# Optimization experiments

Measured on AMD Instinct MI355X. Metric: run time of the kernel, lower is better.

## Reference

```python
import jax, jax.numpy as jnp
import numpy as np

LOG2 = float(np.log(2.0))

def ssp(x):
    # ShiftedSoftplus: softplus(x) - log(2)
    return jax.nn.softplus(x) - LOG2

B, N, F, R, P = 8, 1000, 128, 20, 512000  # batch, atoms, n_atom_basis=n_filters, n_rbf, n_pairs

def setup_inputs() -> dict:
    key = jax.random.key(0)
    ks = jax.random.split(key, 14)
    inv = lambda d: 1.0 / np.sqrt(d)
    return {
        "x": jax.random.normal(ks[0], (B, N, F), dtype=jnp.float32),
        "f_ij": jax.random.normal(ks[1], (P, R), dtype=jnp.float32),
        "idx_i": jax.random.randint(ks[2], (P,), 0, B * N, dtype=jnp.int32),
        "idx_j": jax.random.randint(ks[3], (P,), 0, B * N, dtype=jnp.int32),
        "rcut_ij": jax.random.uniform(ks[4], (P,), dtype=jnp.float32),
        # input_to_feature: Linear(F, F)
        "W_in": jax.random.normal(ks[5], (F, F), dtype=jnp.float32) * inv(F),
        "b_in": jnp.zeros((F,), dtype=jnp.float32),
        # filter_network: Linear(R, F) -> SSP -> Linear(F, F)
        "Wf1": jax.random.normal(ks[6], (R, F), dtype=jnp.float32) * inv(R),
        "bf1": jnp.zeros((F,), dtype=jnp.float32),
        "Wf2": jax.random.normal(ks[7], (F, F), dtype=jnp.float32) * inv(F),
        "bf2": jnp.zeros((F,), dtype=jnp.float32),
        # feature_to_output: Linear(F, F) -> SSP -> Linear(F, F)
        "Wo1": jax.random.normal(ks[8], (F, F), dtype=jnp.float32) * inv(F),
        "bo1": jnp.zeros((F,), dtype=jnp.float32),
        "Wo2": jax.random.normal(ks[9], (F, F), dtype=jnp.float32) * inv(F),
        "bo2": jnp.zeros((F,), dtype=jnp.float32),
    }

def reference(x, f_ij, idx_i, idx_j, rcut_ij,
              W_in, b_in, Wf1, bf1, Wf2, bf2, Wo1, bo1, Wo2, bo2):
    batch, n_atoms = x.shape[0], x.shape[1]
    # input_to_feature
    h = (x @ W_in + b_in).reshape(batch * n_atoms, -1)      # [B*N, F]
    # filter network on radial basis, modulated by cutoff
    Wij = ssp(f_ij @ Wf1 + bf1) @ Wf2 + bf2                 # [P, F]
    Wij = Wij * rcut_ij[:, None]
    # gather neighbor features, elementwise filter, scatter-add to center atom
    x_ij = h[idx_j] * Wij                                   # [P, F]
    agg = jax.ops.segment_sum(x_ij, idx_i, num_segments=batch * n_atoms)  # [B*N, F]
    # feature_to_output
    out = ssp(agg @ Wo1 + bo1) @ Wo2 + bo2
    return out.reshape(batch, n_atoms, 128)
```

## Files before the change

kernel.cpp:

```cpp
#include <hip/hip_runtime.h>
#include <math.h>

#define FDIM 128
#define RDIM 20
#define BN   8000
#define NPAIR 512000
#define PB   64
#define ROWS 8

typedef __attribute__((ext_vector_type(8))) short short8v;
typedef __attribute__((ext_vector_type(4))) float float4v;

__device__ __forceinline__ float sspf_fast(float x) {
    return fmaxf(x, 0.0f) + __logf(1.0f + __expf(-fabsf(x))) - 0.69314718055994531f;
}
__device__ __forceinline__ float sspf(float x) {
    return fmaxf(x, 0.0f) + log1pf(expf(-fabsf(x))) - 0.69314718055994531f;
}

__device__ __forceinline__ unsigned short f2bf(float x) {
    union { float f; unsigned u; } v; v.f = x;
    unsigned r = (v.u + 0x7FFFu + ((v.u >> 16) & 1u)) >> 16;
    return (unsigned short)r;
}

__global__ __launch_bounds__(256) void hist_kernel(
    const int* __restrict__ idx_i, int* __restrict__ cnt)
{
    const int p = blockIdx.x * 256 + threadIdx.x;
    if (p < NPAIR) atomicAdd(&cnt[idx_i[p]], 1);
}

__global__ __launch_bounds__(1024) void scan_kernel(
    const int* __restrict__ cnt, int* __restrict__ cursor)
{
    __shared__ int part[1024];
    const int t = threadIdx.x;
    int v[8]; int sum = 0;
    #pragma unroll
    for (int k = 0; k < 8; ++k) {
        const int i = t * 8 + k;
        const int c = (i < BN) ? cnt[i] : 0;
        v[k] = sum; sum += c;
    }
    part[t] = sum;
    __syncthreads();
    for (int off = 1; off < 1024; off <<= 1) {
        const int x = (t >= off) ? part[t - off] : 0;
        __syncthreads();
        part[t] += x;
        __syncthreads();
    }
    const int base = (t == 0) ? 0 : part[t - 1];
    #pragma unroll
    for (int k = 0; k < 8; ++k) {
        const int i = t * 8 + k;
        if (i < BN) cursor[i] = base + v[k];
    }
}

__global__ __launch_bounds__(256) void scatter_kernel(
    const int* __restrict__ idx_i, int* __restrict__ cursor, int* __restrict__ perm)
{
    const int p = blockIdx.x * 256 + threadIdx.x;
    if (p < NPAIR) {
        const int pos = atomicAdd(&cursor[idx_i[p]], 1);
        perm[pos] = p;
    }
}

template<bool SSP, bool BF16OUT>
__global__ __launch_bounds__(256) void rowgemm_kernel(
    const float* __restrict__ A, const float* __restrict__ W,
    const float* __restrict__ bias, void* __restrict__ Cv)
{
    __shared__ float rowlds[16 * 128];
    const int tid = threadIdx.x;
    const int blk = blockIdx.x;
    for (int s = tid; s < 16 * 128; s += 256)
        rowlds[s] = A[blk * 16 * 128 + s];
    __syncthreads();

    const int lane = tid & 63;
    const int wave = tid >> 6;
    const float b0 = bias[lane];
    const float b1 = bias[64 + lane];
    float acc[4][2];
    #pragma unroll
    for (int rr = 0; rr < 4; ++rr) { acc[rr][0] = b0; acc[rr][1] = b1; }

    #pragma unroll 4
    for (int m = 0; m < 128; ++m) {
        const float w0 = W[m * 128 + lane];
        const float w1 = W[m * 128 + 64 + lane];
        #pragma unroll
        for (int rr = 0; rr < 4; ++rr) {
            const float av = rowlds[(wave * 4 + rr) * 128 + m];
            acc[rr][0] = fmaf(av, w0, acc[rr][0]);
            acc[rr][1] = fmaf(av, w1, acc[rr][1]);
        }
    }

    #pragma unroll
    for (int rr = 0; rr < 4; ++rr) {
        const int p = blk * 16 + wave * 4 + rr;
        float v0 = acc[rr][0], v1 = acc[rr][1];
        if (SSP) { v0 = sspf(v0); v1 = sspf(v1); }
        if (BF16OUT) {
            unsigned short* C = (unsigned short*)Cv;
            C[p * 128 + lane]      = f2bf(v0);
            C[p * 128 + 64 + lane] = f2bf(v1);
        } else {
            float* C = (float*)Cv;
            C[p * 128 + lane]      = v0;
            C[p * 128 + 64 + lane] = v1;
        }
    }
}

__global__ __launch_bounds__(256) void pairs_mfma_agg(
    const float* __restrict__ f_ij, const int* __restrict__ idx_i,
    const int* __restrict__ idx_j, const float* __restrict__ rcut,
    const float* __restrict__ Wf1, const float* __restrict__ bf1,
    const float* __restrict__ Wf2, const float* __restrict__ bf2,
    const unsigned short* __restrict__ h2, const int* __restrict__ rowEnd,
    const int* __restrict__ perm, float* __restrict__ agg)
{
    __shared__ unsigned short xt[64 * 128];
    __shared__ int   rrs[PB];
    __shared__ int   jjs[PB];
    __shared__ float rcs[PB];

    const int tid = threadIdx.x;
    const int w   = tid >> 6;
    const int l   = tid & 63;
    const int l15 = l & 15;
    const int l4  = l >> 4;
    const int swz = (l15 & 7) << 4;

    const int row0 = blockIdx.x * ROWS;
    const int s0 = (row0 == 0) ? 0 : rowEnd[row0 - 1];
    const int s1 = rowEnd[row0 + ROWS - 1];

    short8v wf1a[2];
    #pragma unroll
    for (int kt2 = 0; kt2 < 2; ++kt2) {
        const int ck = w * 32 + kt2 * 16 + l15;
        #pragma unroll
        for (int e = 0; e < 8; ++e) {
            const int r = l4 * 8 + e;
            const float val = (r < RDIM) ? Wf1[r * 128 + ck] : 0.0f;
            wf1a[kt2][e] = (short)f2bf(val);
        }
    }
    short8v wf2a[2][4];
    #pragma unroll
    for (int mt = 0; mt < 2; ++mt) {
        const int c = w * 32 + mt * 16 + l15;
        #pragma unroll
        for (int ks = 0; ks < 4; ++ks) {
            #pragma unroll
            for (int e = 0; e < 8; ++e) {
                const int k = ks * 32 + l4 * 8 + e;
                wf2a[mt][ks][e] = (short)f2bf(Wf2[k * 128 + c]);
            }
        }
    }
    float b1v[2][4], b2v[2][4];
    #pragma unroll
    for (int t = 0; t < 2; ++t)
        #pragma unroll
        for (int j = 0; j < 4; ++j) {
            b1v[t][j] = bf1[w * 32 + t * 16 + l4 * 4 + j];
            b2v[t][j] = bf2[w * 32 + t * 16 + l4 * 4 + j];
        }

    float4v accD[2];
    accD[0] = float4v{0.f, 0.f, 0.f, 0.f};
    accD[1] = float4v{0.f, 0.f, 0.f, 0.f};

    for (int s = s0; s < s1; s += PB) {
        __syncthreads();

        if (tid < PB) {
            const int q  = s + tid;
            const int qc = q < s1 ? q : s1 - 1;
            const int pid = perm[qc];
            rrs[tid] = idx_i[pid] - row0;
            jjs[tid] = idx_j[pid];
            rcs[tid] = (q < s1) ? rcut[pid] : 0.0f;
        }

        short8v ffr[4];
        #pragma unroll
        for (int nt = 0; nt < 4; ++nt) {
            const int q = s + nt * 16 + l15;
            const int pid = perm[q < s1 ? q : s1 - 1];
            const float* fb = &f_ij[(size_t)pid * RDIM];
            float4 fa = {0.f, 0.f, 0.f, 0.f}, fc = {0.f, 0.f, 0.f, 0.f};
            if (l4 < 3) fa = *(const float4*)(fb + l4 * 8);
            if (l4 < 2) fc = *(const float4*)(fb + l4 * 8 + 4);
            ffr[nt][0] = (short)f2bf(fa.x); ffr[nt][1] = (short)f2bf(fa.y);
            ffr[nt][2] = (short)f2bf(fa.z); ffr[nt][3] = (short)f2bf(fa.w);
            ffr[nt][4] = (short)f2bf(fc.x); ffr[nt][5] = (short)f2bf(fc.y);
            ffr[nt][6] = (short)f2bf(fc.z); ffr[nt][7] = (short)f2bf(fc.w);
        }
        __syncthreads();

        unsigned long long hvb[4][2];
        #pragma unroll
        for (int nt = 0; nt < 4; ++nt) {
            const int gj = jjs[nt * 16 + l15] << 7;
            hvb[nt][0] = *(const unsigned long long*)&h2[gj + w * 32 + l4 * 4];
            hvb[nt][1] = *(const unsigned long long*)&h2[gj + w * 32 + 16 + l4 * 4];
        }

        #pragma unroll
        for (int kt2 = 0; kt2 < 2; ++kt2) {
            #pragma unroll
            for (int nt = 0; nt < 4; ++nt) {
                float4v acc1 = {0.f, 0.f, 0.f, 0.f};
                acc1 = __builtin_amdgcn_mfma_f32_16x16x32_bf16(wf1a[kt2], ffr[nt], acc1, 0, 0, 0);
                unsigned short pk[4];
                #pragma unroll
                for (int j = 0; j < 4; ++j)
                    pk[j] = f2bf(sspf_fast(acc1[j] + b1v[kt2][j]));
                const int row = nt * 16 + l15;
                const int byte = row * 256 + ((w * 64 + kt2 * 32 + l4 * 8) ^ swz);
                *(unsigned long long*)((char*)xt + byte) =
                    (unsigned long long)pk[0] | ((unsigned long long)pk[1] << 16) |
                    ((unsigned long long)pk[2] << 32) | ((unsigned long long)pk[3] << 48);
            }
        }
        __syncthreads();

        float4v a2[2][4];
        #pragma unroll
        for (int mt = 0; mt < 2; ++mt)
            #pragma unroll
            for (int nt = 0; nt < 4; ++nt)
                a2[mt][nt] = float4v{0.f, 0.f, 0.f, 0.f};

        #pragma unroll
        for (int ks = 0; ks < 4; ++ks) {
            short8v bfr[4];
            #pragma unroll
            for (int nt = 0; nt < 4; ++nt) {
                const int row = nt * 16 + l15;
                const int byte = row * 256 + ((ks * 64 + l4 * 16) ^ swz);
                bfr[nt] = *(const short8v*)((const char*)xt + byte);
            }
            #pragma unroll
            for (int mt = 0; mt < 2; ++mt)
                #pragma unroll
                for (int nt = 0; nt < 4; ++nt)
                    a2[mt][nt] = __builtin_amdgcn_mfma_f32_16x16x32_bf16(
                        wf2a[mt][ks], bfr[nt], a2[mt][nt], 0, 0, 0);
        }
        __syncthreads();

        #pragma unroll
        for (int nt = 0; nt < 4; ++nt) {
            const int p = nt * 16 + l15;
            const float r = rcs[p];
            #pragma unroll
            for (int mt = 0; mt < 2; ++mt) {
                #pragma unroll
                for (int j = 0; j < 4; ++j) {
                    const int c = w * 32 + mt * 16 + l4 * 4 + j;
                    const float hf = __uint_as_float(
                        (unsigned)((hvb[nt][mt] >> (16 * j)) & 0xFFFFULL) << 16);
                    const float xv = hf * ((a2[mt][nt][j] + b2v[mt][j]) * r);
                    const int byte = c * 128 + ((p * 2) ^ ((c & 7) << 4));
                    *(unsigned short*)((char*)xt + byte) = f2bf(xv);
                }
            }
        }
        __syncthreads();

        #pragma unroll
        for (int ks = 0; ks < 2; ++ks) {
            short8v sfr;
            #pragma unroll
            for (int e = 0; e < 8; ++e) {
                const int pr = ks * 32 + l4 * 8 + e;
                sfr[e] = (rrs[pr] == l15) ? (short)0x3F80 : (short)0;
            }
            #pragma unroll
            for (int mt = 0; mt < 2; ++mt) {
                const int c = w * 32 + mt * 16 + l15;
                const int byte = c * 128 + ((ks * 64 + l4 * 16) ^ swz);
                const short8v xfr = *(const short8v*)((const char*)xt + byte);
                accD[mt] = __builtin_amdgcn_mfma_f32_16x16x32_bf16(xfr, sfr, accD[mt], 0, 0, 0);
            }
        }
    }

    if (l15 < ROWS) {
        #pragma unroll
        for (int mt = 0; mt < 2; ++mt) {
            float4 v;
            v.x = accD[mt][0]; v.y = accD[mt][1]; v.z = accD[mt][2]; v.w = accD[mt][3];
            *(float4*)&agg[(size_t)(row0 + l15) * 128 + w * 32 + mt * 16 + l4 * 4] = v;
        }
    }
}

extern "C" void kernel_launch(void* const* d_in, const int* in_sizes, int n_in,
                              void* d_out, int out_size, void* d_ws, size_t ws_size,
                              hipStream_t stream) {
    const float* x     = (const float*)d_in[0];
    const float* f_ij  = (const float*)d_in[1];
    const int*   idx_i = (const int*)  d_in[2];
    const int*   idx_j = (const int*)  d_in[3];
    const float* rcut  = (const float*)d_in[4];
    const float* W_in  = (const float*)d_in[5];
    const float* b_in  = (const float*)d_in[6];
    const float* Wf1   = (const float*)d_in[7];
    const float* bf1   = (const float*)d_in[8];
    const float* Wf2   = (const float*)d_in[9];
    const float* bf2   = (const float*)d_in[10];
    const float* Wo1   = (const float*)d_in[11];
    const float* bo1   = (const float*)d_in[12];
    const float* Wo2   = (const float*)d_in[13];
    const float* bo2   = (const float*)d_in[14];
    float* out = (float*)d_out;

    unsigned short* h2 = (unsigned short*)d_ws;
    float* agg = (float*)((char*)d_ws + 2048000);
    float* t1  = (float*)((char*)d_ws + 2048000 + 4096000);
    int* perm   = (int*)t1;
    int* cnt    = (int*)((char*)t1 + (size_t)NPAIR * 4);
    int* cursor = cnt + 8001;

    hipMemsetAsync(cnt, 0, (BN + 1) * sizeof(int), stream);
    hist_kernel<<<NPAIR / 256, 256, 0, stream>>>(idx_i, cnt);
    scan_kernel<<<1, 1024, 0, stream>>>(cnt, cursor);
    scatter_kernel<<<NPAIR / 256, 256, 0, stream>>>(idx_i, cursor, perm);

    rowgemm_kernel<false, true><<<BN / 16, 256, 0, stream>>>(x, W_in, b_in, h2);

    pairs_mfma_agg<<<BN / ROWS, 256, 0, stream>>>(
        f_ij, idx_i, idx_j, rcut, Wf1, bf1, Wf2, bf2, h2, cursor, perm, agg);

    rowgemm_kernel<true,  false><<<BN / 16, 256, 0, stream>>>(agg, Wo1, bo1, t1);
    rowgemm_kernel<false, false><<<BN / 16, 256, 0, stream>>>(t1, Wo2, bo2, out);
}
```

Before: 238.0 us.

## Split pair-kernel LDS buffers, drop barriers, restructure filter loop, use packed bf16 conversion

The pair kernel now uses separate LDS buffers for the filter activations and the gathered products. Because each wave reads only the product columns it wrote itself, two __syncthreads per tile can be removed. The second filter GEMM now loops over the output tile outer-most, gathering h2 per tile, so fewer accumulators and neighbour values are live at once. Launch bounds request 4 blocks per CU. The hand-written bf16 rounding is replaced with the HIP intrinsic conversions, including a packed two-value variant. The trade-off is higher LDS use per block, which may limit how many blocks actually fit per CU.

```diff
diff --git a/kernel.cpp b/kernel.cpp
--- a/kernel.cpp
+++ b/kernel.cpp
@@ -1,4 +1,5 @@
 #include <hip/hip_runtime.h>
+#include <hip/hip_bf16.h>
 #include <math.h>
 
 #define FDIM 128
@@ -18,10 +19,15 @@
     return fmaxf(x, 0.0f) + log1pf(expf(-fabsf(x))) - 0.69314718055994531f;
 }
 
-__device__ __forceinline__ unsigned short f2bf(float x) {
-    union { float f; unsigned u; } v; v.f = x;
-    unsigned r = (v.u + 0x7FFFu + ((v.u >> 16) & 1u)) >> 16;
-    return (unsigned short)r;
+__device__ __forceinline__ unsigned short bfs(float a) {
+    union { __hip_bfloat16 h; unsigned short u; } v;
+    v.h = __float2bfloat16(a);
+    return v.u;
+}
+__device__ __forceinline__ unsigned pkbf(float a, float b) {
+    union { __hip_bfloat162 h; unsigned u; } v;
+    v.h = __float22bfloat162_rn(make_float2(a, b));
+    return v.u;
 }
 
 __global__ __launch_bounds__(256) void hist_kernel(
@@ -108,8 +114,8 @@
         if (SSP) { v0 = sspf(v0); v1 = sspf(v1); }
         if (BF16OUT) {
             unsigned short* C = (unsigned short*)Cv;
-            C[p * 128 + lane]      = f2bf(v0);
-            C[p * 128 + 64 + lane] = f2bf(v1);
+            C[p * 128 + lane]      = bfs(v0);
+            C[p * 128 + 64 + lane] = bfs(v1);
         } else {
             float* C = (float*)Cv;
             C[p * 128 + lane]      = v0;
@@ -118,7 +124,7 @@
     }
 }
 
-__global__ __launch_bounds__(256) void pairs_mfma_agg(
+__global__ __launch_bounds__(256, 4) void pairs_v7(
     const float* __restrict__ f_ij, const int* __restrict__ idx_i,
     const int* __restrict__ idx_j, const float* __restrict__ rcut,
     const float* __restrict__ Wf1, const float* __restrict__ bf1,
@@ -126,7 +132,8 @@
     const unsigned short* __restrict__ h2, const int* __restrict__ rowEnd,
     const int* __restrict__ perm, float* __restrict__ agg)
 {
-    __shared__ unsigned short xt[64 * 128];
+    __shared__ unsigned short act[64 * 128];
+    __shared__ unsigned short xbuf[128 * 64];
     __shared__ int   rrs[PB];
     __shared__ int   jjs[PB];
     __shared__ float rcs[PB];
@@ -150,7 +157,7 @@
         for (int e = 0; e < 8; ++e) {
             const int r = l4 * 8 + e;
             const float val = (r < RDIM) ? Wf1[r * 128 + ck] : 0.0f;
-            wf1a[kt2][e] = (short)f2bf(val);
+            wf1a[kt2][e] = (short)bfs(val);
         }
     }
     short8v wf2a[2][4];
@@ -162,7 +169,7 @@
             #pragma unroll
             for (int e = 0; e < 8; ++e) {
                 const int k = ks * 32 + l4 * 8 + e;
-                wf2a[mt][ks][e] = (short)f2bf(Wf2[k * 128 + c]);
+                wf2a[mt][ks][e] = (short)bfs(Wf2[k * 128 + c]);
             }
         }
     }
@@ -200,20 +207,12 @@
             float4 fa = {0.f, 0.f, 0.f, 0.f}, fc = {0.f, 0.f, 0.f, 0.f};
             if (l4 < 3) fa = *(const float4*)(fb + l4 * 8);
             if (l4 < 2) fc = *(const float4*)(fb + l4 * 8 + 4);
-            ffr[nt][0] = (short)f2bf(fa.x); ffr[nt][1] = (short)f2bf(fa.y);
-            ffr[nt][2] = (short)f2bf(fa.z); ffr[nt][3] = (short)f2bf(fa.w);
-            ffr[nt][4] = (short)f2bf(fc.x); ffr[nt][5] = (short)f2bf(fc.y);
-            ffr[nt][6] = (short)f2bf(fc.z); ffr[nt][7] = (short)f2bf(fc.w);
-        }
-        __syncthreads();
-
-        unsigned long long hvb[4][2];
-        #pragma unroll
-        for (int nt = 0; nt < 4; ++nt) {
-            const int gj = jjs[nt * 16 + l15] << 7;
-            hvb[nt][0] = *(const unsigned long long*)&h2[gj + w * 32 + l4 * 4];
-            hvb[nt][1] = *(const unsigned long long*)&h2[gj + w * 32 + 16 + l4 * 4];
-        }
+            union { unsigned u[4]; short8v v; } pk;
+            pk.u[0] = pkbf(fa.x, fa.y); pk.u[1] = pkbf(fa.z, fa.w);
+            pk.u[2] = pkbf(fc.x, fc.y); pk.u[3] = pkbf(fc.z, fc.w);
+            ffr[nt] = pk.v;
+        }
+        __syncthreads();
 
         #pragma unroll
         for (int kt2 = 0; kt2 < 2; ++kt2) {
@@ -221,62 +220,64 @@
             for (int nt = 0; nt < 4; ++nt) {
                 float4v acc1 = {0.f, 0.f, 0.f, 0.f};
                 acc1 = __builtin_amdgcn_mfma_f32_16x16x32_bf16(wf1a[kt2], ffr[nt], acc1, 0, 0, 0);
-                unsigned short pk[4];
-                #pragma unroll
-                for (int j = 0; j < 4; ++j)
-                    pk[j] = f2bf(sspf_fast(acc1[j] + b1v[kt2][j]));
+                const unsigned lo = pkbf(sspf_fast(acc1[0] + b1v[kt2][0]),
+                                         sspf_fast(acc1[1] + b1v[kt2][1]));
+                const unsigned hi = pkbf(sspf_fast(acc1[2] + b1v[kt2][2]),
+                                         sspf_fast(acc1[3] + b1v[kt2][3]));
                 const int row = nt * 16 + l15;
                 const int byte = row * 256 + ((w * 64 + kt2 * 32 + l4 * 8) ^ swz);
-                *(unsigned long long*)((char*)xt + byte) =
-                    (unsigned long long)pk[0] | ((unsigned long long)pk[1] << 16) |
-                    ((unsigned long long)pk[2] << 32) | ((unsigned long long)pk[3] << 48);
-            }
-        }
-        __syncthreads();
-
-        float4v a2[2][4];
-        #pragma unroll
-        for (int mt = 0; mt < 2; ++mt)
-            #pragma unroll
-            for (int nt = 0; nt < 4; ++nt)
-                a2[mt][nt] = float4v{0.f, 0.f, 0.f, 0.f};
-
-        #pragma unroll
-        for (int ks = 0; ks < 4; ++ks) {
-            short8v bfr[4];
+                *(unsigned long long*)((char*)act + byte) =
+                    (unsigned long long)lo | ((unsigned long long)hi << 32);
+            }
+        }
+        __syncthreads();
+
+        #pragma unroll
+        for (int mt = 0; mt < 2; ++mt) {
+            unsigned long long hv[4];
             #pragma unroll
             for (int nt = 0; nt < 4; ++nt) {
-                const int row = nt * 16 + l15;
-                const int byte = row * 256 + ((ks * 64 + l4 * 16) ^ swz);
-                bfr[nt] = *(const short8v*)((const char*)xt + byte);
-            }
-            #pragma unroll
-            for (int mt = 0; mt < 2; ++mt)
+                const int gj = jjs[nt * 16 + l15] << 7;
+                hv[nt] = *(const unsigned long long*)&h2[gj + w * 32 + mt * 16 + l4 * 4];
+            }
+
+            float4v a2[4];
+            #pragma unroll
+            for (int nt = 0; nt < 4; ++nt) a2[nt] = float4v{0.f, 0.f, 0.f, 0.f};
+
+            #pragma unroll
+            for (int ks = 0; ks < 4; ++ks) {
+                short8v bfr[4];
+                #pragma unroll
+                for (int nt = 0; nt < 4; ++nt) {
+                    const int row = nt * 16 + l15;
+                    const int byte = row * 256 + ((ks * 64 + l4 * 16) ^ swz);
+                    bfr[nt] = *(const short8v*)((const char*)act + byte);
+                }
                 #pragma unroll
                 for (int nt = 0; nt < 4; ++nt)
-                    a2[mt][nt] = __builtin_amdgcn_mfma_f32_16x16x32_bf16(
-                        wf2a[mt][ks], bfr[nt], a2[mt][nt], 0, 0, 0);
-        }
-        __syncthreads();
-
-        #pragma unroll
-        for (int nt = 0; nt < 4; ++nt) {
-            const int p = nt * 16 + l15;
-            const float r = rcs[p];
-            #pragma unroll
-            for (int mt = 0; mt < 2; ++mt) {
+                    a2[nt] = __builtin_amdgcn_mfma_f32_16x16x32_bf16(
+                        wf2a[mt][ks], bfr[nt], a2[nt], 0, 0, 0);
+            }
+
+            #pragma unroll
+            for (int nt = 0; nt < 4; ++nt) {
+                const int p = nt * 16 + l15;
+                const float r = rcs[p];
+                const unsigned lo = (unsigned)hv[nt];
+                const unsigned hi = (unsigned)(hv[nt] >> 32);
+                const float hf[4] = {
+                    __uint_as_float(lo << 16), __uint_as_float(lo & 0xFFFF0000u),
+                    __uint_as_float(hi << 16), __uint_as_float(hi & 0xFFFF0000u) };
                 #pragma unroll
                 for (int j = 0; j < 4; ++j) {
                     const int c = w * 32 + mt * 16 + l4 * 4 + j;
-                    const float hf = __uint_as_float(
-                        (unsigned)((hvb[nt][mt] >> (16 * j)) & 0xFFFFULL) << 16);
-                    const float xv = hf * ((a2[mt][nt][j] + b2v[mt][j]) * r);
+                    const float xv = hf[j] * ((a2[nt][j] + b2v[mt][j]) * r);
                     const int byte = c * 128 + ((p * 2) ^ ((c & 7) << 4));
-                    *(unsigned short*)((char*)xt + byte) = f2bf(xv);
+                    *(unsigned short*)((char*)xbuf + byte) = bfs(xv);
                 }
             }
         }
-        __syncthreads();
 
         #pragma unroll
         for (int ks = 0; ks < 2; ++ks) {
@@ -290,7 +291,7 @@
             for (int mt = 0; mt < 2; ++mt) {
                 const int c = w * 32 + mt * 16 + l15;
                 const int byte = c * 128 + ((ks * 64 + l4 * 16) ^ swz);
-                const short8v xfr = *(const short8v*)((const char*)xt + byte);
+                const short8v xfr = *(const short8v*)((const char*)xbuf + byte);
                 accD[mt] = __builtin_amdgcn_mfma_f32_16x16x32_bf16(xfr, sfr, accD[mt], 0, 0, 0);
             }
         }
@@ -340,7 +341,7 @@
 
     rowgemm_kernel<false, true><<<BN / 16, 256, 0, stream>>>(x, W_in, b_in, h2);
 
-    pairs_mfma_agg<<<BN / ROWS, 256, 0, stream>>>(
+    pairs_v7<<<BN / ROWS, 256, 0, stream>>>(
         f_ij, idx_i, idx_j, rcut, Wf1, bf1, Wf2, bf2, h2, cursor, perm, agg);
 
     rowgemm_kernel<true,  false><<<BN / 16, 256, 0, stream>>>(agg, Wo1, bo1, t1);
```

New measurement: 306.1 us. 1.29x slower.
